# Kernel tuning notes

Hardware: AMD Instinct MI355X
Metric: run time of the kernel (lower is better)

Reference implementation:

```python
import jax, jax.numpy as jnp
import numpy as np

NHEAD = 8
EPS = 1e-5


def ln(x, g, b):
    m = x.mean(-1, keepdims=True)
    v = ((x - m) ** 2).mean(-1, keepdims=True)
    return (x - m) * jax.lax.rsqrt(v + EPS) * g + b


def mha_rel(q_in, kv_in, pos_enc, pos_idx, Wqkv, bqkv, Wo, bo):
    # q_in, kv_in: [W, N, C] where N = hn*bs
    w, n, c = q_in.shape
    hd = c // NHEAD
    Wq, Wk, Wv = Wqkv[:c], Wqkv[c:2 * c], Wqkv[2 * c:]
    bq, bk, bv = bqkv[:c], bqkv[c:2 * c], bqkv[2 * c:]
    q = q_in @ Wq.T + bq
    k = kv_in @ Wk.T + bk
    v = kv_in @ Wv.T + bv
    # relative position lookup: [2W-1,1,C] gathered by flat [W*W] -> [W,W,C]
    pe = pos_enc[pos_idx].reshape(w, w, c)
    q_r = pe @ Wq.T + bq
    k_r = pe @ Wk.T + bk
    scale = hd ** -0.5
    q = (q * scale).reshape(w, n, NHEAD, hd)
    q_r = (q_r * scale).reshape(w, w, NHEAD, hd)
    k = k.reshape(w, n, NHEAD, hd)
    v = v.reshape(w, n, NHEAD, hd)
    k_r = k_r.reshape(w, w, NHEAD, hd)
    # content-content + content-pos + pos-content scores: [N, E, W, W']
    attn = (jnp.einsum('wnec,vnec->newv', q, k)
            + jnp.einsum('wnec,wvec->newv', q, k_r)
            + jnp.einsum('vnec,wvec->newv', k, q_r))
    raw = attn
    a = jax.nn.softmax(attn, axis=-1)
    vo = jnp.einsum('newv,vnec->wnec', a, v).reshape(w, n, c)
    vo = vo @ Wo.T + bo
    return vo, raw.sum(axis=1)  # [W,N,C], [N,W,W]


def setup_inputs() -> dict:
    key = jax.random.key(0)
    bs, c, hn, w = 2, 128, 64, 256
    ks = jax.random.split(key, 5)
    feat_left = jax.random.normal(ks[0], (bs, c, hn, w), jnp.float32)
    feat_right = jax.random.normal(ks[1], (bs, c, hn, w), jnp.float32)
    pos = jax.random.normal(ks[2], (2 * w - 1, 1, c), jnp.float32)
    r = jnp.arange(w)
    pos_indexes = (r[:, None] - r[None, :] + w - 1).reshape(-1).astype(jnp.int32)
    Wqkv = jax.random.normal(ks[3], (3 * c, c), jnp.float32) * 0.02
    bqkv = jnp.zeros((3 * c,), jnp.float32)
    Wo = jax.random.normal(ks[4], (c, c), jnp.float32) * 0.02
    bo = jnp.zeros((c,), jnp.float32)
    g1 = jnp.ones((c,), jnp.float32)
    b1 = jnp.zeros((c,), jnp.float32)
    g2 = jnp.ones((c,), jnp.float32)
    b2 = jnp.zeros((c,), jnp.float32)
    return dict(feat_left=feat_left, feat_right=feat_right, pos=pos,
                pos_indexes=pos_indexes, Wqkv=Wqkv, bqkv=bqkv, Wo=Wo, bo=bo,
                g1=g1, b1=b1, g2=g2, b2=b2)


def reference(feat_left, feat_right, pos, pos_indexes, Wqkv, bqkv, Wo, bo, g1, b1, g2, b2):
    bs, c, hn, w = feat_left.shape

    def to_seq(f):  # [bs,c,hn,w] -> [w, hn*bs, c]
        return jnp.transpose(f, (1, 3, 2, 0)).reshape(c, w, hn * bs).transpose(1, 2, 0)

    fl = to_seq(feat_left)
    fr = to_seq(feat_right)
    fl2 = ln(fl, g1, b1)
    fr2 = ln(fr, g1, b1)
    # right attends to left with flipped relative pos enc
    upd_r, _ = mha_rel(fr2, fl2, jnp.flip(pos, axis=0), pos_indexes, Wqkv, bqkv, Wo, bo)
    fr = fr + upd_r
    # left attends to updated right (last_layer=False -> no causal mask)
    fr2 = ln(fr, g2, b2)
    upd_l, raw = mha_rel(fl2, fr2, pos, pos_indexes, Wqkv, bqkv, Wo, bo)
    fl = fl + upd_l
    raw_attn = raw.reshape(hn, bs, w, w).transpose(1, 0, 2, 3)  # [bs,hn,w,w]

    def from_seq(f):  # [w, hn*bs, c] -> [bs,c,hn,w]
        return f.reshape(w, hn, bs, c).transpose(2, 3, 1, 0)

    return from_seq(fl), from_seq(fr), raw_attn
```

## Files before the change

### kernel.cpp

```cpp
#include <hip/hip_runtime.h>
#include <cstddef>

static constexpr int Wd  = 256;
static constexpr int NBd = 128;
static constexpr int Cd  = 128;
static constexpr int BSd = 2;
static constexpr int HNd = 64;
static constexpr size_t SEQF = (size_t)Wd * NBd * Cd;

typedef __attribute__((ext_vector_type(8))) short bf16x8;
typedef __attribute__((ext_vector_type(4))) short bf16x4;
typedef __attribute__((ext_vector_type(4))) float f32x4;
typedef __attribute__((ext_vector_type(2))) float f32x2;

__device__ inline short f2bf(float f) {
  union { float f; unsigned u; } v; v.f = f;
  return (short)((v.u + 0x7FFFu + ((v.u >> 16) & 1u)) >> 16);
}

__global__ __launch_bounds__(256) void k_to_seq_ln(
    const float* __restrict__ fA, const float* __restrict__ fB,
    float* __restrict__ seqA, float* __restrict__ seqB,
    short* __restrict__ lnA, short* __restrict__ lnB,
    const float* __restrict__ g, const float* __restrict__ bb) {
  __shared__ float red[2][8][33];
  __shared__ float mv[2][32];
  const int z = blockIdx.y;
  const float* feat = (z < 128) ? fA : fB;
  float* seq = (z < 128) ? seqA : seqB;
  short* lno = (z < 128) ? lnA : lnB;
  const int hb = z & 127;
  const int h = hb >> 1, b = hb & 1;
  const int n = h * BSd + b;
  const int w0 = blockIdx.x * 32;
  const int t = threadIdx.x;
  const int wl = t & 31, cg = t >> 5, c0 = cg * 16;
  float v[16];
  float s1 = 0.f, s2 = 0.f;
#pragma unroll
  for (int r = 0; r < 16; ++r) {
    v[r] = feat[(((size_t)b * Cd + c0 + r) * HNd + h) * Wd + w0 + wl];
    s1 += v[r]; s2 += v[r] * v[r];
  }
  red[0][cg][wl] = s1; red[1][cg][wl] = s2;
  __syncthreads();
  if (t < 32) {
    float a1 = 0.f, a2 = 0.f;
#pragma unroll
    for (int k = 0; k < 8; ++k) { a1 += red[0][k][t]; a2 += red[1][k][t]; }
    float mean = a1 * (1.0f / Cd);
    float var = a2 * (1.0f / Cd) - mean * mean;
    mv[0][t] = mean; mv[1][t] = rsqrtf(var + 1e-5f);
  }
  __syncthreads();
  const float mean = mv[0][wl], rstd = mv[1][wl];
  float* so = &seq[((size_t)(w0 + wl) * NBd + n) * Cd + c0];
  short* bo_ = &lno[((size_t)(w0 + wl) * NBd + n) * Cd + c0];
#pragma unroll
  for (int r = 0; r < 16; ++r) so[r] = v[r];
#pragma unroll
  for (int r = 0; r < 16; ++r)
    bo_[r] = f2bf((v[r] - mean) * rstd * g[c0 + r] + bb[c0 + r]);
}

__global__ __launch_bounds__(256) void k_from_seq2(const float* __restrict__ seqA,
                                                   const float* __restrict__ seqB,
                                                   float* __restrict__ featA,
                                                   float* __restrict__ featB) {
  __shared__ float tile[32][33];
  int wi0 = blockIdx.x * 32, ci0 = blockIdx.y * 32;
  int z = blockIdx.z;
  const float* seq = (z < 128) ? seqA : seqB;
  float* feat = (z < 128) ? featA : featB;
  int hb = z & 127;
  int h = hb >> 1, b = hb & 1;
  int n = h * BSd + b;
  int tx = threadIdx.x, ty = threadIdx.y;
#pragma unroll
  for (int r = 0; r < 4; ++r) {
    int wi = wi0 + ty + r * 8;
    tile[ty + r * 8][tx] = seq[((size_t)wi * NBd + n) * Cd + ci0 + tx];
  }
  __syncthreads();
#pragma unroll
  for (int r = 0; r < 4; ++r) {
    int ci = ci0 + ty + r * 8;
    feat[(((size_t)b * Cd + ci) * HNd + h) * Wd + wi0 + tx] = tile[tx][ty + r * 8];
  }
}

__global__ __launch_bounds__(256) void k_cvt(const float* __restrict__ w1, short* d1,
                                             const float* __restrict__ w2, short* d2,
                                             const float* __restrict__ w3, short* d3)
{
  int i = blockIdx.x * 256 + threadIdx.x;
  if (i < 49152) d1[i] = f2bf(w1[i]);
  if (i < 16384) d2[i] = f2bf(w2[i]);
  if (i < 65408) d3[i] = f2bf(w3[i]);
}

__global__ __launch_bounds__(256) void k_gemm_bf(
    const short* __restrict__ A, const short* __restrict__ Wt,
    const float* __restrict__ bias, float* __restrict__ outF,
    short* __restrict__ outB, int M, int ldout, int scaleN0, float scale,
    const short* __restrict__ A2, short* __restrict__ outB2, int ldout2, int yCut) {
  const int t = threadIdx.x;
  const int lane = t & 63, wv = t >> 6;
  const int ml = lane & 15, quad = lane >> 4;
  const int m0 = blockIdx.x * 64;
  int yb = blockIdx.y;
  const short* Ap = A;
  short* oB = outB;
  float* oF = outF;
  int ld = ldout;
  int nblk = yb;
  if (yb >= yCut) { Ap = A2; oB = outB2; oF = nullptr; ld = ldout2; nblk = 0; }
  const int n0 = nblk * 128 + wv * 32;
  const bf16x8 zero8 = {0, 0, 0, 0, 0, 0, 0, 0};

  bf16x8 Bfr[2][4];
#pragma unroll
  for (int nf = 0; nf < 2; ++nf)
#pragma unroll
    for (int ks = 0; ks < 4; ++ks)
      Bfr[nf][ks] = *(const bf16x8*)&Wt[(size_t)(n0 + nf * 16 + ml) * 128 + ks * 32 + quad * 8];

  f32x4 acc[4][2];
#pragma unroll
  for (int mf = 0; mf < 4; ++mf)
#pragma unroll
    for (int nf = 0; nf < 2; ++nf) acc[mf][nf] = {0.f, 0.f, 0.f, 0.f};

#pragma unroll
  for (int ks = 0; ks < 4; ++ks) {
    bf16x8 Af[4];
#pragma unroll
    for (int mf = 0; mf < 4; ++mf) {
      int m = m0 + mf * 16 + ml;
      Af[mf] = (m < M) ? *(const bf16x8*)&Ap[(size_t)m * 128 + ks * 32 + quad * 8] : zero8;
    }
#pragma unroll
    for (int mf = 0; mf < 4; ++mf)
#pragma unroll
      for (int nf = 0; nf < 2; ++nf)
        acc[mf][nf] = __builtin_amdgcn_mfma_f32_16x16x32_bf16(Af[mf], Bfr[nf][ks], acc[mf][nf], 0, 0, 0);
  }

#pragma unroll
  for (int nf = 0; nf < 2; ++nf) {
    int n = n0 + nf * 16 + ml;
    float bi = bias[n];
    float sc = (n < scaleN0) ? scale : 1.0f;
#pragma unroll
    for (int mf = 0; mf < 4; ++mf) {
#pragma unroll
      for (int r = 0; r < 4; ++r) {
        int m = m0 + mf * 16 + quad * 4 + r;
        if (m >= M) continue;
        float v = (acc[mf][nf][r] + bi) * sc;
        if (oF) oF[(size_t)m * ld + n] = v;
        if (oB) oB[(size_t)m * ld + n] = f2bf(v);
      }
    }
  }
}

__global__ __launch_bounds__(256) void k_gemm_wo_ln(
    const short* __restrict__ A, const short* __restrict__ Wt,
    const float* __restrict__ bias, const float* __restrict__ res,
    float* __restrict__ outF, short* __restrict__ outLN,
    const float* __restrict__ lng, const float* __restrict__ lnb) {
  const int t = threadIdx.x;
  const int lane = t & 63, wv = t >> 6;
  const int ml = lane & 15, quad = lane >> 4;
  const int m0 = blockIdx.x * 64 + wv * 16;
  const int ii = m0 >> 7;
  const int nn = (m0 & 127) + ml;

  f32x4 acc[8];
#pragma unroll
  for (int nf = 0; nf < 8; ++nf) acc[nf] = {0.f, 0.f, 0.f, 0.f};
#pragma unroll
  for (int ks = 0; ks < 4; ++ks) {
    bf16x8 Af = *(const bf16x8*)&A[(((size_t)nn * 8 + ks * 2 + (quad >> 1)) * 256 + ii) * 16 +
                                   (quad & 1) * 8];
#pragma unroll
    for (int nf = 0; nf < 8; ++nf) {
      bf16x8 Bf = *(const bf16x8*)&Wt[(size_t)(nf * 16 + ml) * 128 + ks * 32 + quad * 8];
      acc[nf] = __builtin_amdgcn_mfma_f32_16x16x32_bf16(Af, Bf, acc[nf], 0, 0, 0);
    }
  }
  float val[8][4];
#pragma unroll
  for (int nf = 0; nf < 8; ++nf) {
    float bi = bias[nf * 16 + ml];
#pragma unroll
    for (int r = 0; r < 4; ++r) {
      int m = m0 + quad * 4 + r;
      val[nf][r] = acc[nf][r] + bi + res[(size_t)m * 128 + nf * 16 + ml];
      outF[(size_t)m * 128 + nf * 16 + ml] = val[nf][r];
    }
  }
  if (outLN) {
#pragma unroll
    for (int r = 0; r < 4; ++r) {
      float s1 = 0.f, s2 = 0.f;
#pragma unroll
      for (int nf = 0; nf < 8; ++nf) { s1 += val[nf][r]; s2 += val[nf][r] * val[nf][r]; }
#pragma unroll
      for (int mk = 1; mk < 16; mk <<= 1) { s1 += __shfl_xor(s1, mk); s2 += __shfl_xor(s2, mk); }
      float mean = s1 * (1.0f / 128.f);
      float var = s2 * (1.0f / 128.f) - mean * mean;
      float rstd = rsqrtf(var + 1e-5f);
      int m = m0 + quad * 4 + r;
#pragma unroll
      for (int nf = 0; nf < 8; ++nf) {
        int nn2 = nf * 16 + ml;
        outLN[(size_t)m * 128 + nn2] = f2bf((val[nf][r] - mean) * rstd * lng[nn2] + lnb[nn2]);
      }
    }
  }
}

template <int PASS>
__global__ __launch_bounds__(256, 3) void k_attn_mfma(
    const short* __restrict__ Qg, int ldq,
    const short* __restrict__ Kg, const short* __restrict__ Vg, int ldkv,
    const short* __restrict__ PP, short* __restrict__ OT) {
  __shared__ short Ks[256][16];
  __shared__ short VTs[16][264];
  __shared__ float R2T[4][2][16][20];

  const int t = threadIdx.x;
  const int n = blockIdx.x;
  const int e = blockIdx.y;
  const int lane = t & 63, wv = t >> 6;
  const int ml = lane & 15, quad = lane >> 4;
  const bool lo = lane < 32;
  const bf16x8 zero8 = {0, 0, 0, 0, 0, 0, 0, 0};
  const f32x4 z4 = {0.f, 0.f, 0.f, 0.f};

#pragma unroll
  for (int it = 0; it < 4; ++it) {
    int idx = t + it * 256;
    int r = idx >> 2, c4 = idx & 3;
    *(bf16x4*)&Ks[r][c4 * 4] =
        *(const bf16x4*)&Kg[((size_t)r * NBd + n) * ldkv + e * 16 + c4 * 4];
  }
#pragma unroll
  for (int it = 0; it < 4; ++it) {
    bf16x4 vv = *(const bf16x4*)&Vg[((size_t)t * NBd + n) * ldkv + e * 16 + it * 4];
    VTs[it * 4 + 0][t] = vv[0];
    VTs[it * 4 + 1][t] = vv[1];
    VTs[it * 4 + 2][t] = vv[2];
    VTs[it * 4 + 3][t] = vv[3];
  }
  __syncthreads();

  const int pbase = (PASS == 2) ? (ml - quad * 4 + 15) : (quad * 4 - ml + 15);
  const int qsh = quad << 6;

  const short* PPe = PP + e * 16;
  short* OTb = OT + (size_t)(n * 8 + e) * 256 * 16;

  for (int ipl = 0; ipl < 2; ++ipl) {
    const int i0p = ((int)blockIdx.z * 2 + ipl) * 64;
    const int wb = (PASS == 2) ? i0p : (192 - i0p);
    bf16x8 bQ = lo ? *(const bf16x8*)&Qg[((size_t)(i0p + 16 * wv + ml) * NBd + n) * ldq +
                                         e * 16 + quad * 8]
                   : zero8;
    f32x4 Ot = {0.f, 0.f, 0.f, 0.f};
    float den = 0.f;

    bf16x8 fPQprev;
    {
      int pp = (PASS == 2) ? (wb + 16 * wv + 256 + ml) : (wb - 16 * wv + 48 + ml);
      if (pp > 510) pp = 510;
      const short* pr = &PPe[(size_t)pp * 256];
      bf16x8 fPK0 = lo ? *(const bf16x8*)&pr[128 + quad * 8] : zero8;
      fPQprev     = lo ? *(const bf16x8*)&pr[quad * 8] : zero8;
      f32x4 R2i = __builtin_amdgcn_mfma_f32_16x16x32_bf16(bQ, fPK0, z4, 0, 0, 0);
      *(f32x4*)&R2T[wv][1][ml][quad * 4] = R2i;
    }
    bf16x8 fPK, fPQf;
    {
      int pf = (PASS == 2) ? (wb + 16 * wv + 240 + ml) : (wb - 16 * wv + 64 + ml);
      if (pf > 510) pf = 510;
      const short* prf = &PPe[(size_t)pf * 256];
      fPK  = lo ? *(const bf16x8*)&prf[128 + quad * 8] : zero8;
      fPQf = lo ? *(const bf16x8*)&prf[quad * 8] : zero8;
    }

    f32x4 St_p, R3a_p, R3b_p;
    unsigned pA0 = 0, pA1 = 0;
    bf16x8 aKn;

    {
      bf16x8 aK = lo ? *(const bf16x8*)&Ks[ml][quad * 8] : zero8;
      St_p = __builtin_amdgcn_mfma_f32_16x16x32_bf16(aK, bQ, z4, 0, 0, 0);
      f32x4 R2c = __builtin_amdgcn_mfma_f32_16x16x32_bf16(bQ, fPK, z4, 0, 0, 0);
      if (PASS == 2) {
        R3a_p = __builtin_amdgcn_mfma_f32_16x16x32_bf16(aK, fPQf, z4, 0, 0, 0);
        R3b_p = __builtin_amdgcn_mfma_f32_16x16x32_bf16(aK, fPQprev, z4, 0, 0, 0);
      } else {
        R3b_p = __builtin_amdgcn_mfma_f32_16x16x32_bf16(aK, fPQf, z4, 0, 0, 0);
        R3a_p = __builtin_amdgcn_mfma_f32_16x16x32_bf16(aK, fPQprev, z4, 0, 0, 0);
      }
      fPQprev = fPQf;
      {
        int pf = (PASS == 2) ? (wb + 16 * wv - 16 + 240 + ml) : (wb - 16 * wv + 16 + 64 + ml);
        if (pf > 510) pf = 510;
        const short* prf = &PPe[(size_t)pf * 256];
        fPK  = lo ? *(const bf16x8*)&prf[128 + quad * 8] : zero8;
        fPQf = lo ? *(const bf16x8*)&prf[quad * 8] : zero8;
      }
      aKn = lo ? *(const bf16x8*)&Ks[16 + ml][quad * 8] : zero8;
      *(f32x4*)&R2T[wv][0][ml][quad * 4] = R2c;
    }

#pragma unroll
    for (int i = 1; i < 16; ++i) {
      const int T = i - 1;
      const int j0 = i * 16;

      float r2v[4], va[4], vb[4];
#pragma unroll
      for (int r = 0; r < 4; ++r) {
        const int pcol = (PASS == 2) ? (pbase - r) : (pbase + r);
        const int hi = pcol >> 4;
        const int bk = (T & 1) ^ hi ^ (PASS == 1 ? 1 : 0);
        const int ba = ((pcol & 15) << 2) | qsh;
        r2v[r] = R2T[wv][bk][pcol & 15][ml];
        va[r] = __int_as_float(
            __builtin_amdgcn_ds_bpermute(ba, __float_as_int(R3a_p[r])));
        vb[r] = __int_as_float(
            __builtin_amdgcn_ds_bpermute(ba, __float_as_int(R3b_p[r])));
      }
      bf16x8 aVT = zero8;
      if (T & 1) aVT = *(const bf16x8*)&VTs[ml][(T >> 1) * 32 + quad * 8];

      bf16x8 aK = aKn;
      f32x4 St_c = __builtin_amdgcn_mfma_f32_16x16x32_bf16(aK, bQ, z4, 0, 0, 0);
      f32x4 R2c  = __builtin_amdgcn_mfma_f32_16x16x32_bf16(bQ, fPK, z4, 0, 0, 0);
      f32x4 R3A, R3B;
      if (PASS == 2) {
        R3A = __builtin_amdgcn_mfma_f32_16x16x32_bf16(aK, fPQf, z4, 0, 0, 0);
        R3B = __builtin_amdgcn_mfma_f32_16x16x32_bf16(aK, fPQprev, z4, 0, 0, 0);
      } else {
        R3B = __builtin_amdgcn_mfma_f32_16x16x32_bf16(aK, fPQf, z4, 0, 0, 0);
        R3A = __builtin_amdgcn_mfma_f32_16x16x32_bf16(aK, fPQprev, z4, 0, 0, 0);
      }
      fPQprev = fPQf;
      if (i < 15) {
        int pf = (PASS == 2) ? (wb + 16 * wv - (j0 + 16) + 240 + ml)
                             : (wb - 16 * wv + (j0 + 16) + 64 + ml);
        if (pf > 510) pf = 510;
        const short* prf = &PPe[(size_t)pf * 256];
        fPK  = lo ? *(const bf16x8*)&prf[128 + quad * 8] : zero8;
        fPQf = lo ? *(const bf16x8*)&prf[quad * 8] : zero8;
        aKn = lo ? *(const bf16x8*)&Ks[j0 + 16 + ml][quad * 8] : zero8;
      }

      float pe4[4];
#pragma unroll
      for (int r = 0; r < 4; ++r) {
        const int pcol = (PASS == 2) ? (pbase - r) : (pbase + r);
        const int hi = pcol >> 4;
        float s = St_p[r] + r2v[r] + (hi ? vb[r] : va[r]);
        pe4[r] = __expf(s);
        den += pe4[r];
      }
      unsigned d0, d1;
      asm("v_cvt_pk_bf16_f32 %0, %1, %2" : "=v"(d0) : "v"(pe4[0]), "v"(pe4[1]));
      asm("v_cvt_pk_bf16_f32 %0, %1, %2" : "=v"(d1) : "v"(pe4[2]), "v"(pe4[3]));
      if ((T & 1) == 0) {
        pA0 = d0;
        pA1 = d1;
      } else {
        unsigned b0 = pA0, b2 = d0, b1 = pA1, b3 = d1;
        asm("v_permlane32_swap_b32 %0, %1" : "+v"(b0), "+v"(b2));
        asm("v_permlane16_swap_b32 %0, %1" : "+v"(b0), "+v"(b2));
        asm("v_permlane32_swap_b32 %0, %1" : "+v"(b1), "+v"(b3));
        asm("v_permlane16_swap_b32 %0, %1" : "+v"(b1), "+v"(b3));
        union { unsigned u[4]; bf16x8 v8; } bp;
        bp.u[0] = b0; bp.u[1] = b1; bp.u[2] = b2; bp.u[3] = b3;
        Ot = __builtin_amdgcn_mfma_f32_16x16x32_bf16(aVT, bp.v8, Ot, 0, 0, 0);
      }
      *(f32x4*)&R2T[wv][i & 1][ml][quad * 4] = R2c;
      St_p = St_c; R3a_p = R3A; R3b_p = R3B;
    }

    {
      const int T = 15;
      float r2v[4], va[4], vb[4];
#pragma unroll
      for (int r = 0; r < 4; ++r) {
        const int pcol = (PASS == 2) ? (pbase - r) : (pbase + r);
        const int hi = pcol >> 4;
        const int bk = (T & 1) ^ hi ^ (PASS == 1 ? 1 : 0);
        const int ba = ((pcol & 15) << 2) | qsh;
        r2v[r] = R2T[wv][bk][pcol & 15][ml];
        va[r] = __int_as_float(
            __builtin_amdgcn_ds_bpermute(ba, __float_as_int(R3a_p[r])));
        vb[r] = __int_as_float(
            __builtin_amdgcn_ds_bpermute(ba, __float_as_int(R3b_p[r])));
      }
      bf16x8 aVT = *(const bf16x8*)&VTs[ml][(T >> 1) * 32 + quad * 8];
      float pe4[4];
#pragma unroll
      for (int r = 0; r < 4; ++r) {
        const int pcol = (PASS == 2) ? (pbase - r) : (pbase + r);
        const int hi = pcol >> 4;
        float s = St_p[r] + r2v[r] + (hi ? vb[r] : va[r]);
        pe4[r] = __expf(s);
        den += pe4[r];
      }
      unsigned d0, d1;
      asm("v_cvt_pk_bf16_f32 %0, %1, %2" : "=v"(d0) : "v"(pe4[0]), "v"(pe4[1]));
      asm("v_cvt_pk_bf16_f32 %0, %1, %2" : "=v"(d1) : "v"(pe4[2]), "v"(pe4[3]));
      unsigned b0 = pA0, b2 = d0, b1 = pA1, b3 = d1;
      asm("v_permlane32_swap_b32 %0, %1" : "+v"(b0), "+v"(b2));
      asm("v_permlane16_swap_b32 %0, %1" : "+v"(b0), "+v"(b2));
      asm("v_permlane32_swap_b32 %0, %1" : "+v"(b1), "+v"(b3));
      asm("v_permlane16_swap_b32 %0, %1" : "+v"(b1), "+v"(b3));
      union { unsigned u[4]; bf16x8 v8; } bp;
      bp.u[0] = b0; bp.u[1] = b1; bp.u[2] = b2; bp.u[3] = b3;
      Ot = __builtin_amdgcn_mfma_f32_16x16x32_bf16(aVT, bp.v8, Ot, 0, 0, 0);
    }

    den += __shfl_xor(den, 16);
    den += __shfl_xor(den, 32);
    float inv = 1.f / den;
    bf16x4 ob;
    ob[0] = f2bf(Ot[0] * inv); ob[1] = f2bf(Ot[1] * inv);
    ob[2] = f2bf(Ot[2] * inv); ob[3] = f2bf(Ot[3] * inv);
    *(bf16x4*)&OTb[(size_t)(i0p + 16 * wv + ml) * 16 + quad * 4] = ob;
  }
}

__global__ __launch_bounds__(256, 4) void k_raw(
    const short* __restrict__ Qf, const short* __restrict__ Kf,
    const short* __restrict__ PP, float* __restrict__ raw) {
  __shared__ float R2s[4][2][16][17];
  __shared__ float R3s[4][16][34];
  const int t = threadIdx.x;
  const int n = blockIdx.y;
  const int lane = t & 63, wv = t >> 6;
  const int ml = lane & 15, quad = lane >> 4;
  const int it0 = blockIdx.x * 64 + wv * 16;
  const int jt0 = blockIdx.z * 4;
  const f32x4 z4 = {0.f, 0.f, 0.f, 0.f};

  bf16x8 aQ[4];
#pragma unroll
  for (int kc = 0; kc < 4; ++kc)
    aQ[kc] = *(const bf16x8*)&Qf[((size_t)(it0 + ml) * NBd + n) * 384 + kc * 32 + quad * 8];

  float* rbase = &raw[(((size_t)(n & 1) * HNd + (n >> 1)) * Wd + it0) * Wd];

  bf16x8 fPQprev[4];
  {
    int pp = it0 - jt0 * 16 + 256 + ml;
    if (pp > 510) pp = 510;
    const short* pr = &PP[(size_t)pp * 256];
    f32x4 R2i = z4;
#pragma unroll
    for (int kc = 0; kc < 4; ++kc) {
      bf16x8 fPK = *(const bf16x8*)&pr[128 + kc * 32 + quad * 8];
      R2i = __builtin_amdgcn_mfma_f32_16x16x32_bf16(aQ[kc], fPK, R2i, 0, 0, 0);
      fPQprev[kc] = *(const bf16x8*)&pr[kc * 32 + quad * 8];
    }
#pragma unroll
    for (int r = 0; r < 4; ++r) R2s[wv][1][quad * 4 + r][ml] = R2i[r];
  }

#pragma unroll
  for (int jq = 0; jq < 4; ++jq) {
    const int j0 = (jt0 + jq) * 16;
    bf16x8 aK[4];
#pragma unroll
    for (int kc = 0; kc < 4; ++kc)
      aK[kc] = *(const bf16x8*)&Kf[((size_t)(j0 + ml) * NBd + n) * 256 + kc * 32 + quad * 8];
    const int p0 = it0 - j0 + 240 + ml;
    const short* pr0 = &PP[(size_t)p0 * 256];
    f32x4 St = z4, R2f = z4, R3a = z4, R3b = z4;
    bf16x8 fPQ0[4];
#pragma unroll
    for (int kc = 0; kc < 4; ++kc)
      St = __builtin_amdgcn_mfma_f32_16x16x32_bf16(aQ[kc], aK[kc], St, 0, 0, 0);
#pragma unroll
    for (int kc = 0; kc < 4; ++kc) {
      bf16x8 fPK0 = *(const bf16x8*)&pr0[128 + kc * 32 + quad * 8];
      R2f = __builtin_amdgcn_mfma_f32_16x16x32_bf16(aQ[kc], fPK0, R2f, 0, 0, 0);
    }
#pragma unroll
    for (int kc = 0; kc < 4; ++kc) {
      fPQ0[kc] = *(const bf16x8*)&pr0[kc * 32 + quad * 8];
      R3a = __builtin_amdgcn_mfma_f32_16x16x32_bf16(aK[kc], fPQ0[kc], R3a, 0, 0, 0);
    }
#pragma unroll
    for (int kc = 0; kc < 4; ++kc)
      R3b = __builtin_amdgcn_mfma_f32_16x16x32_bf16(aK[kc], fPQprev[kc], R3b, 0, 0, 0);
#pragma unroll
    for (int kc = 0; kc < 4; ++kc) fPQprev[kc] = fPQ0[kc];
#pragma unroll
    for (int r = 0; r < 4; ++r) {
      R2s[wv][jq & 1][quad * 4 + r][ml] = R2f[r];
      R3s[wv][quad * 4 + r][ml]      = R3a[r];
      R3s[wv][quad * 4 + r][ml + 16] = R3b[r];
    }
#pragma unroll
    for (int r = 0; r < 4; ++r) {
      const int il = quad * 4 + r;
      const int pcol = il - ml + 15;
      const int hi = pcol >> 4, col = pcol & 15;
      const int bk = (jq & 1) ^ hi;
      rbase[(size_t)il * Wd + j0 + ml] = St[r] + R2s[wv][bk][il][col] + R3s[wv][ml][pcol];
    }
  }
}

extern "C" void kernel_launch(void* const* d_in, const int* in_sizes, int n_in,
                              void* d_out, int out_size, void* d_ws, size_t ws_size,
                              hipStream_t stream) {
  const float* feat_l = (const float*)d_in[0];
  const float* feat_r = (const float*)d_in[1];
  const float* pos    = (const float*)d_in[2];
  const float* Wqkv = (const float*)d_in[4];
  const float* bqkv = (const float*)d_in[5];
  const float* Wo   = (const float*)d_in[6];
  const float* bo   = (const float*)d_in[7];
  const float* g1   = (const float*)d_in[8];
  const float* b1   = (const float*)d_in[9];
  const float* g2   = (const float*)d_in[10];
  const float* b2   = (const float*)d_in[11];
  float* out = (float*)d_out;

  float* ws = (float*)d_ws;
  float* fl_seq = ws;
  float* fr_seq = ws + SEQF;
  float* fr2_f  = ws + 2 * SEQF;
  float* fl_new = ws + 3 * SEQF;
  short* wsb    = (short*)(ws + 4 * SEQF);
  short* fl2_b   = wsb;
  short* fr2_b   = wsb + SEQF;
  short* frb2_b  = wsb + 2 * SEQF;
  short* QKVl_b  = wsb + 3 * SEQF;
  short* Qr_b    = wsb + 6 * SEQF;
  short* KVr2_b  = wsb + 7 * SEQF;
  short* O_b     = wsb + 9 * SEQF;
  short* PP_b    = wsb + 10 * SEQF;
  short* Wb      = PP_b + 131072;
  short* pos_b   = Wb + 65536;

  k_to_seq_ln<<<dim3(8, 256), 256, 0, stream>>>(feat_l, feat_r, fl_seq, fr_seq,
                                                fl2_b, fr2_b, g1, b1);
  k_cvt<<<256, 256, 0, stream>>>(Wqkv, Wb, Wo, Wb + 49152, pos, pos_b);

  k_gemm_bf<<<dim3(8, 2), 256, 0, stream>>>(pos_b, Wb, bqkv, nullptr, PP_b,
                                            511, 256, 128, 0.25f,
                                            nullptr, nullptr, 0, 999);
  k_gemm_bf<<<dim3(512, 4), 256, 0, stream>>>(fl2_b, Wb, bqkv, nullptr, QKVl_b,
                                              32768, 384, 128, 0.25f,
                                              fr2_b, Qr_b, 128, 3);

  k_attn_mfma<1><<<dim3(128, 8, 2), 256, 0, stream>>>(
      Qr_b, Cd, QKVl_b + 128, QKVl_b + 256, 384, PP_b, O_b);
  k_gemm_wo_ln<<<512, 256, 0, stream>>>(O_b, Wb + 49152, bo, fr_seq, fr2_f,
                                        frb2_b, g2, b2);
  k_gemm_bf<<<dim3(512, 2), 256, 0, stream>>>(frb2_b, Wb + 16384, bqkv + 128, nullptr,
                                              KVr2_b, 32768, 256, 0, 1.0f,
                                              nullptr, nullptr, 0, 999);
  k_attn_mfma<2><<<dim3(128, 8, 2), 256, 0, stream>>>(
      QKVl_b, 384, KVr2_b, KVr2_b + 128, 256, PP_b, O_b);
  k_raw<<<dim3(4, 128, 4), 256, 0, stream>>>(QKVl_b, KVr2_b, PP_b, out + 2 * SEQF);
  k_gemm_wo_ln<<<512, 256, 0, stream>>>(O_b, Wb + 49152, bo, fl_seq, fl_new,
                                        nullptr, nullptr, nullptr);

  k_from_seq2<<<dim3(8, 4, 256), dim3(32, 8), 0, stream>>>(fl_new, fr2_f, out, out + SEQF);

  (void)in_sizes; (void)n_in; (void)out_size; (void)ws_size;
}
```

Measured before the change: 390.9 us.

## Software-pipeline k_raw tiles with prefetch and transposed LDS staging

Restructures the raw-score kernel into a software pipeline: the K and positional fragments for the next 16-column tile are prefetched into registers while the current tile's MFMAs run, and the combine-and-store of the previous tile is deferred so it overlaps the current MFMAs. The LDS staging buffers are transposed and padded so each lane writes its accumulators as one f32x4 vector, and R3 is double-buffered. The added live registers force a drop in launch bounds from 4 to 3 waves per SIMD, which trades occupancy for latency hiding.

Result: no change. 390.3 us (-0.1%).

```diff
diff --git a/kernel.cpp b/kernel.cpp
--- a/kernel.cpp
+++ b/kernel.cpp
@@ -438,11 +438,11 @@
   }
 }
 
-__global__ __launch_bounds__(256, 4) void k_raw(
+__global__ __launch_bounds__(256, 3) void k_raw(
     const short* __restrict__ Qf, const short* __restrict__ Kf,
     const short* __restrict__ PP, float* __restrict__ raw) {
-  __shared__ float R2s[4][2][16][17];
-  __shared__ float R3s[4][16][34];
+  __shared__ float R2T[4][2][16][20];
+  __shared__ float R3T[4][2][32][20];
   const int t = threadIdx.x;
   const int n = blockIdx.y;
   const int lane = t & 63, wv = t >> 6;
@@ -470,52 +470,123 @@
       R2i = __builtin_amdgcn_mfma_f32_16x16x32_bf16(aQ[kc], fPK, R2i, 0, 0, 0);
       fPQprev[kc] = *(const bf16x8*)&pr[kc * 32 + quad * 8];
     }
-#pragma unroll
-    for (int r = 0; r < 4; ++r) R2s[wv][1][quad * 4 + r][ml] = R2i[r];
-  }
-
-#pragma unroll
-  for (int jq = 0; jq < 4; ++jq) {
-    const int j0 = (jt0 + jq) * 16;
-    bf16x8 aK[4];
-#pragma unroll
-    for (int kc = 0; kc < 4; ++kc)
-      aK[kc] = *(const bf16x8*)&Kf[((size_t)(j0 + ml) * NBd + n) * 256 + kc * 32 + quad * 8];
+    *(f32x4*)&R2T[wv][1][ml][quad * 4] = R2i;
+  }
+
+  bf16x8 aKn[4], fPKn[4], fPQn[4];
+  {
+    const int j0 = jt0 * 16;
+#pragma unroll
+    for (int kc = 0; kc < 4; ++kc)
+      aKn[kc] = *(const bf16x8*)&Kf[((size_t)(j0 + ml) * NBd + n) * 256 + kc * 32 + quad * 8];
     const int p0 = it0 - j0 + 240 + ml;
     const short* pr0 = &PP[(size_t)p0 * 256];
+#pragma unroll
+    for (int kc = 0; kc < 4; ++kc) {
+      fPKn[kc] = *(const bf16x8*)&pr0[128 + kc * 32 + quad * 8];
+      fPQn[kc] = *(const bf16x8*)&pr0[kc * 32 + quad * 8];
+    }
+  }
+
+  f32x4 St_p;
+  {
     f32x4 St = z4, R2f = z4, R3a = z4, R3b = z4;
-    bf16x8 fPQ0[4];
-#pragma unroll
-    for (int kc = 0; kc < 4; ++kc)
-      St = __builtin_amdgcn_mfma_f32_16x16x32_bf16(aQ[kc], aK[kc], St, 0, 0, 0);
+#pragma unroll
+    for (int kc = 0; kc < 4; ++kc)
+      St = __builtin_amdgcn_mfma_f32_16x16x32_bf16(aQ[kc], aKn[kc], St, 0, 0, 0);
+#pragma unroll
+    for (int kc = 0; kc < 4; ++kc)
+      R2f = __builtin_amdgcn_mfma_f32_16x16x32_bf16(aQ[kc], fPKn[kc], R2f, 0, 0, 0);
+#pragma unroll
+    for (int kc = 0; kc < 4; ++kc)
+      R3a = __builtin_amdgcn_mfma_f32_16x16x32_bf16(aKn[kc], fPQn[kc], R3a, 0, 0, 0);
+#pragma unroll
+    for (int kc = 0; kc < 4; ++kc)
+      R3b = __builtin_amdgcn_mfma_f32_16x16x32_bf16(aKn[kc], fPQprev[kc], R3b, 0, 0, 0);
+#pragma unroll
+    for (int kc = 0; kc < 4; ++kc) fPQprev[kc] = fPQn[kc];
+    *(f32x4*)&R2T[wv][0][ml][quad * 4] = R2f;
+    *(f32x4*)&R3T[wv][0][ml][quad * 4] = R3a;
+    *(f32x4*)&R3T[wv][0][ml + 16][quad * 4] = R3b;
+    St_p = St;
+    const int j0n = (jt0 + 1) * 16;
+#pragma unroll
+    for (int kc = 0; kc < 4; ++kc)
+      aKn[kc] = *(const bf16x8*)&Kf[((size_t)(j0n + ml) * NBd + n) * 256 + kc * 32 + quad * 8];
+    const int p0n = it0 - j0n + 240 + ml;
+    const short* prn = &PP[(size_t)p0n * 256];
 #pragma unroll
     for (int kc = 0; kc < 4; ++kc) {
-      bf16x8 fPK0 = *(const bf16x8*)&pr0[128 + kc * 32 + quad * 8];
-      R2f = __builtin_amdgcn_mfma_f32_16x16x32_bf16(aQ[kc], fPK0, R2f, 0, 0, 0);
-    }
-#pragma unroll
-    for (int kc = 0; kc < 4; ++kc) {
-      fPQ0[kc] = *(const bf16x8*)&pr0[kc * 32 + quad * 8];
-      R3a = __builtin_amdgcn_mfma_f32_16x16x32_bf16(aK[kc], fPQ0[kc], R3a, 0, 0, 0);
-    }
-#pragma unroll
-    for (int kc = 0; kc < 4; ++kc)
-      R3b = __builtin_amdgcn_mfma_f32_16x16x32_bf16(aK[kc], fPQprev[kc], R3b, 0, 0, 0);
-#pragma unroll
-    for (int kc = 0; kc < 4; ++kc) fPQprev[kc] = fPQ0[kc];
-#pragma unroll
-    for (int r = 0; r < 4; ++r) {
-      R2s[wv][jq & 1][quad * 4 + r][ml] = R2f[r];
-      R3s[wv][quad * 4 + r][ml]      = R3a[r];
-      R3s[wv][quad * 4 + r][ml + 16] = R3b[r];
-    }
+      fPKn[kc] = *(const bf16x8*)&prn[128 + kc * 32 + quad * 8];
+      fPQn[kc] = *(const bf16x8*)&prn[kc * 32 + quad * 8];
+    }
+  }
+
+#pragma unroll
+  for (int i = 1; i < 4; ++i) {
+    const int T = i - 1;
+    float r2v[4], r3v[4];
 #pragma unroll
     for (int r = 0; r < 4; ++r) {
       const int il = quad * 4 + r;
       const int pcol = il - ml + 15;
       const int hi = pcol >> 4, col = pcol & 15;
-      const int bk = (jq & 1) ^ hi;
-      rbase[(size_t)il * Wd + j0 + ml] = St[r] + R2s[wv][bk][il][col] + R3s[wv][ml][pcol];
+      const int bk = (T & 1) ^ hi;
+      r2v[r] = R2T[wv][bk][col][il];
+      r3v[r] = R3T[wv][T & 1][pcol][ml];
+    }
+    f32x4 St = z4, R2f = z4, R3a = z4, R3b = z4;
+#pragma unroll
+    for (int kc = 0; kc < 4; ++kc)
+      St = __builtin_amdgcn_mfma_f32_16x16x32_bf16(aQ[kc], aKn[kc], St, 0, 0, 0);
+#pragma unroll
+    for (int kc = 0; kc < 4; ++kc)
+      R2f = __builtin_amdgcn_mfma_f32_16x16x32_bf16(aQ[kc], fPKn[kc], R2f, 0, 0, 0);
+#pragma unroll
+    for (int kc = 0; kc < 4; ++kc)
+      R3a = __builtin_amdgcn_mfma_f32_16x16x32_bf16(aKn[kc], fPQn[kc], R3a, 0, 0, 0);
+#pragma unroll
+    for (int kc = 0; kc < 4; ++kc)
+      R3b = __builtin_amdgcn_mfma_f32_16x16x32_bf16(aKn[kc], fPQprev[kc], R3b, 0, 0, 0);
+#pragma unroll
+    for (int kc = 0; kc < 4; ++kc) fPQprev[kc] = fPQn[kc];
+    if (i < 3) {
+      const int j0n = (jt0 + i + 1) * 16;
+#pragma unroll
+      for (int kc = 0; kc < 4; ++kc)
+        aKn[kc] = *(const bf16x8*)&Kf[((size_t)(j0n + ml) * NBd + n) * 256 + kc * 32 + quad * 8];
+      const int p0n = it0 - j0n + 240 + ml;
+      const short* prn = &PP[(size_t)p0n * 256];
+#pragma unroll
+      for (int kc = 0; kc < 4; ++kc) {
+        fPKn[kc] = *(const bf16x8*)&prn[128 + kc * 32 + quad * 8];
+        fPQn[kc] = *(const bf16x8*)&prn[kc * 32 + quad * 8];
+      }
+    }
+    const int j0T = (jt0 + T) * 16;
+#pragma unroll
+    for (int r = 0; r < 4; ++r) {
+      const int il = quad * 4 + r;
+      rbase[(size_t)il * Wd + j0T + ml] = St_p[r] + r2v[r] + r3v[r];
+    }
+    *(f32x4*)&R2T[wv][i & 1][ml][quad * 4] = R2f;
+    *(f32x4*)&R3T[wv][i & 1][ml][quad * 4] = R3a;
+    *(f32x4*)&R3T[wv][i & 1][ml + 16][quad * 4] = R3b;
+    St_p = St;
+  }
+
+  {
+    const int T = 3;
+    const int j0T = (jt0 + T) * 16;
+#pragma unroll
+    for (int r = 0; r < 4; ++r) {
+      const int il = quad * 4 + r;
+      const int pcol = il - ml + 15;
+      const int hi = pcol >> 4, col = pcol & 15;
+      const int bk = (T & 1) ^ hi;
+      float r2v = R2T[wv][bk][col][il];
+      float r3v = R3T[wv][T & 1][pcol][ml];
+      rbase[(size_t)il * Wd + j0T + ml] = St_p[r] + r2v + r3v;
     }
   }
 }
```

## Transpose positional projections for coalesced loads and stage Q/K tiles in LDS for raw scores

Applied to the files above, without the earlier changes.

Adds a small kernel that rearranges the projected positional table into an 8-element-chunk-major layout. Lanes that read consecutive positions then touch contiguous 16-byte chunks instead of rows strided by 256 elements, in both attention passes and the raw-score kernel. The raw-score kernel also stages its 64x128 Q and K tiles in shared memory with coalesced vector loads rather than strided global fragment loads, and its occupancy hint drops from 4 to 3 blocks. The cost is one extra launch, extra workspace, and about 33 KB more LDS per block in the raw kernel.

Measured after the change: 349.6 us. 10.6% less time.

```diff
diff --git a/kernel.cpp b/kernel.cpp
--- a/kernel.cpp
+++ b/kernel.cpp
@@ -99,6 +99,13 @@
   if (i < 65408) d3[i] = f2bf(w3[i]);
 }
 
+__global__ __launch_bounds__(256) void k_ppt(const short* __restrict__ src,
+                                             short* __restrict__ dst) {
+  int row = blockIdx.x;
+  int c = threadIdx.x;
+  dst[((size_t)(c >> 3) * 511 + row) * 8 + (c & 7)] = src[(size_t)row * 256 + c];
+}
+
 __global__ __launch_bounds__(256) void k_gemm_bf(
     const short* __restrict__ A, const short* __restrict__ Wt,
     const float* __restrict__ bias, float* __restrict__ outF,
@@ -226,7 +233,7 @@
 __global__ __launch_bounds__(256, 3) void k_attn_mfma(
     const short* __restrict__ Qg, int ldq,
     const short* __restrict__ Kg, const short* __restrict__ Vg, int ldkv,
-    const short* __restrict__ PP, short* __restrict__ OT) {
+    const short* __restrict__ PPT, short* __restrict__ OT) {
   __shared__ short Ks[256][16];
   __shared__ short VTs[16][264];
   __shared__ float R2T[4][2][16][20];
@@ -260,7 +267,9 @@
   const int pbase = (PASS == 2) ? (ml - quad * 4 + 15) : (quad * 4 - ml + 15);
   const int qsh = quad << 6;
 
-  const short* PPe = PP + e * 16;
+  const short* PQe = PPT + (size_t)(e * 2 + quad) * 511 * 8;
+  const short* PKe = PQe + (size_t)16 * 511 * 8;
+
   short* OTb = OT + (size_t)(n * 8 + e) * 256 * 16;
 
   for (int ipl = 0; ipl < 2; ++ipl) {
@@ -276,9 +285,8 @@
     {
       int pp = (PASS == 2) ? (wb + 16 * wv + 256 + ml) : (wb - 16 * wv + 48 + ml);
       if (pp > 510) pp = 510;
-      const short* pr = &PPe[(size_t)pp * 256];
-      bf16x8 fPK0 = lo ? *(const bf16x8*)&pr[128 + quad * 8] : zero8;
-      fPQprev     = lo ? *(const bf16x8*)&pr[quad * 8] : zero8;
+      bf16x8 fPK0 = lo ? *(const bf16x8*)&PKe[(size_t)pp * 8] : zero8;
+      fPQprev     = lo ? *(const bf16x8*)&PQe[(size_t)pp * 8] : zero8;
       f32x4 R2i = __builtin_amdgcn_mfma_f32_16x16x32_bf16(bQ, fPK0, z4, 0, 0, 0);
       *(f32x4*)&R2T[wv][1][ml][quad * 4] = R2i;
     }
@@ -286,9 +294,8 @@
     {
       int pf = (PASS == 2) ? (wb + 16 * wv + 240 + ml) : (wb - 16 * wv + 64 + ml);
       if (pf > 510) pf = 510;
-      const short* prf = &PPe[(size_t)pf * 256];
-      fPK  = lo ? *(const bf16x8*)&prf[128 + quad * 8] : zero8;
-      fPQf = lo ? *(const bf16x8*)&prf[quad * 8] : zero8;
+      fPK  = lo ? *(const bf16x8*)&PKe[(size_t)pf * 8] : zero8;
+      fPQf = lo ? *(const bf16x8*)&PQe[(size_t)pf * 8] : zero8;
     }
 
     f32x4 St_p, R3a_p, R3b_p;
@@ -310,9 +317,8 @@
       {
         int pf = (PASS == 2) ? (wb + 16 * wv - 16 + 240 + ml) : (wb - 16 * wv + 16 + 64 + ml);
         if (pf > 510) pf = 510;
-        const short* prf = &PPe[(size_t)pf * 256];
-        fPK  = lo ? *(const bf16x8*)&prf[128 + quad * 8] : zero8;
-        fPQf = lo ? *(const bf16x8*)&prf[quad * 8] : zero8;
+        fPK  = lo ? *(const bf16x8*)&PKe[(size_t)pf * 8] : zero8;
+        fPQf = lo ? *(const bf16x8*)&PQe[(size_t)pf * 8] : zero8;
       }
       aKn = lo ? *(const bf16x8*)&Ks[16 + ml][quad * 8] : zero8;
       *(f32x4*)&R2T[wv][0][ml][quad * 4] = R2c;
@@ -355,9 +361,8 @@
         int pf = (PASS == 2) ? (wb + 16 * wv - (j0 + 16) + 240 + ml)
                              : (wb - 16 * wv + (j0 + 16) + 64 + ml);
         if (pf > 510) pf = 510;
-        const short* prf = &PPe[(size_t)pf * 256];
-        fPK  = lo ? *(const bf16x8*)&prf[128 + quad * 8] : zero8;
-        fPQf = lo ? *(const bf16x8*)&prf[quad * 8] : zero8;
+        fPK  = lo ? *(const bf16x8*)&PKe[(size_t)pf * 8] : zero8;
+        fPQf = lo ? *(const bf16x8*)&PQe[(size_t)pf * 8] : zero8;
         aKn = lo ? *(const bf16x8*)&Ks[j0 + 16 + ml][quad * 8] : zero8;
       }
 
@@ -438,37 +443,54 @@
   }
 }
 
-__global__ __launch_bounds__(256, 4) void k_raw(
+__global__ __launch_bounds__(256, 3) void k_raw(
     const short* __restrict__ Qf, const short* __restrict__ Kf,
-    const short* __restrict__ PP, float* __restrict__ raw) {
+    const short* __restrict__ PPT, float* __restrict__ raw) {
   __shared__ float R2s[4][2][16][17];
   __shared__ float R3s[4][16][34];
+  __shared__ short QSs[64][132];
+  __shared__ short KSs[64][132];
   const int t = threadIdx.x;
   const int n = blockIdx.y;
   const int lane = t & 63, wv = t >> 6;
   const int ml = lane & 15, quad = lane >> 4;
-  const int it0 = blockIdx.x * 64 + wv * 16;
+  const int itb = blockIdx.x * 64;
+  const int jtb = blockIdx.z * 64;
+  const int it0 = itb + wv * 16;
   const int jt0 = blockIdx.z * 4;
   const f32x4 z4 = {0.f, 0.f, 0.f, 0.f};
 
+#pragma unroll
+  for (int it = 0; it < 4; ++it) {
+    int idx = t + it * 256;
+    int r = idx >> 4, c8 = idx & 15;
+    *(bf16x8*)&QSs[r][c8 * 8] =
+        *(const bf16x8*)&Qf[((size_t)(itb + r) * NBd + n) * 384 + c8 * 8];
+    *(bf16x8*)&KSs[r][c8 * 8] =
+        *(const bf16x8*)&Kf[((size_t)(jtb + r) * NBd + n) * 256 + c8 * 8];
+  }
+  __syncthreads();
+
   bf16x8 aQ[4];
 #pragma unroll
   for (int kc = 0; kc < 4; ++kc)
-    aQ[kc] = *(const bf16x8*)&Qf[((size_t)(it0 + ml) * NBd + n) * 384 + kc * 32 + quad * 8];
+    aQ[kc] = *(const bf16x8*)&QSs[wv * 16 + ml][kc * 32 + quad * 8];
 
   float* rbase = &raw[(((size_t)(n & 1) * HNd + (n >> 1)) * Wd + it0) * Wd];
+
+  const short* PQb = PPT + (size_t)quad * 511 * 8;
+  const short* PKb = PQb + (size_t)16 * 511 * 8;
 
   bf16x8 fPQprev[4];
   {
     int pp = it0 - jt0 * 16 + 256 + ml;
     if (pp > 510) pp = 510;
-    const short* pr = &PP[(size_t)pp * 256];
     f32x4 R2i = z4;
 #pragma unroll
     for (int kc = 0; kc < 4; ++kc) {
-      bf16x8 fPK = *(const bf16x8*)&pr[128 + kc * 32 + quad * 8];
+      bf16x8 fPK = *(const bf16x8*)&PKb[((size_t)kc * 4 * 511 + pp) * 8];
       R2i = __builtin_amdgcn_mfma_f32_16x16x32_bf16(aQ[kc], fPK, R2i, 0, 0, 0);
-      fPQprev[kc] = *(const bf16x8*)&pr[kc * 32 + quad * 8];
+      fPQprev[kc] = *(const bf16x8*)&PQb[((size_t)kc * 4 * 511 + pp) * 8];
     }
 #pragma unroll
     for (int r = 0; r < 4; ++r) R2s[wv][1][quad * 4 + r][ml] = R2i[r];
@@ -480,9 +502,8 @@
     bf16x8 aK[4];
 #pragma unroll
     for (int kc = 0; kc < 4; ++kc)
-      aK[kc] = *(const bf16x8*)&Kf[((size_t)(j0 + ml) * NBd + n) * 256 + kc * 32 + quad * 8];
+      aK[kc] = *(const bf16x8*)&KSs[jq * 16 + ml][kc * 32 + quad * 8];
     const int p0 = it0 - j0 + 240 + ml;
-    const short* pr0 = &PP[(size_t)p0 * 256];
     f32x4 St = z4, R2f = z4, R3a = z4, R3b = z4;
     bf16x8 fPQ0[4];
 #pragma unroll
@@ -490,12 +511,12 @@
       St = __builtin_amdgcn_mfma_f32_16x16x32_bf16(aQ[kc], aK[kc], St, 0, 0, 0);
 #pragma unroll
     for (int kc = 0; kc < 4; ++kc) {
-      bf16x8 fPK0 = *(const bf16x8*)&pr0[128 + kc * 32 + quad * 8];
+      bf16x8 fPK0 = *(const bf16x8*)&PKb[((size_t)kc * 4 * 511 + p0) * 8];
       R2f = __builtin_amdgcn_mfma_f32_16x16x32_bf16(aQ[kc], fPK0, R2f, 0, 0, 0);
     }
 #pragma unroll
     for (int kc = 0; kc < 4; ++kc) {
-      fPQ0[kc] = *(const bf16x8*)&pr0[kc * 32 + quad * 8];
+      fPQ0[kc] = *(const bf16x8*)&PQb[((size_t)kc * 4 * 511 + p0) * 8];
       R3a = __builtin_amdgcn_mfma_f32_16x16x32_bf16(aK[kc], fPQ0[kc], R3a, 0, 0, 0);
     }
 #pragma unroll
@@ -552,6 +573,7 @@
   short* PP_b    = wsb + 10 * SEQF;
   short* Wb      = PP_b + 131072;
   short* pos_b   = Wb + 65536;
+  short* PPT_b   = pos_b + 65536;
 
   k_to_seq_ln<<<dim3(8, 256), 256, 0, stream>>>(feat_l, feat_r, fl_seq, fr_seq,
                                                 fl2_b, fr2_b, g1, b1);
@@ -560,20 +582,22 @@
   k_gemm_bf<<<dim3(8, 2), 256, 0, stream>>>(pos_b, Wb, bqkv, nullptr, PP_b,
                                             511, 256, 128, 0.25f,
                                             nullptr, nullptr, 0, 999);
+  k_ppt<<<511, 256, 0, stream>>>(PP_b, PPT_b);
+
   k_gemm_bf<<<dim3(512, 4), 256, 0, stream>>>(fl2_b, Wb, bqkv, nullptr, QKVl_b,
                                               32768, 384, 128, 0.25f,
                                               fr2_b, Qr_b, 128, 3);
 
   k_attn_mfma<1><<<dim3(128, 8, 2), 256, 0, stream>>>(
-      Qr_b, Cd, QKVl_b + 128, QKVl_b + 256, 384, PP_b, O_b);
+      Qr_b, Cd, QKVl_b + 128, QKVl_b + 256, 384, PPT_b, O_b);
   k_gemm_wo_ln<<<512, 256, 0, stream>>>(O_b, Wb + 49152, bo, fr_seq, fr2_f,
                                         frb2_b, g2, b2);
   k_gemm_bf<<<dim3(512, 2), 256, 0, stream>>>(frb2_b, Wb + 16384, bqkv + 128, nullptr,
                                               KVr2_b, 32768, 256, 0, 1.0f,
                                               nullptr, nullptr, 0, 999);
   k_attn_mfma<2><<<dim3(128, 8, 2), 256, 0, stream>>>(
-      QKVl_b, 384, KVr2_b, KVr2_b + 128, 256, PP_b, O_b);
-  k_raw<<<dim3(4, 128, 4), 256, 0, stream>>>(QKVl_b, KVr2_b, PP_b, out + 2 * SEQF);
+      QKVl_b, 384, KVr2_b, KVr2_b + 128, 256, PPT_b, O_b);
+  k_raw<<<dim3(4, 128, 4), 256, 0, stream>>>(QKVl_b, KVr2_b, PPT_b, out + 2 * SEQF);
   k_gemm_wo_ln<<<512, 256, 0, stream>>>(O_b, Wb + 49152, bo, fl_seq, fl_new,
                                         nullptr, nullptr, nullptr);
 
```
